# Optimization experiments

Hardware: AMD Instinct MI355X
Metric: run time of the kernel (lower is better)

The kernel has to match this reference:

```python
import jax, jax.numpy as jnp
import numpy as np

N_NODES = 250000
N_EDGES = 8000000


def _gcn_prep(edge_index, n):
    # PyG GCNConv default: add self-loops, symmetric normalization
    row = jnp.concatenate([edge_index[0], jnp.arange(n, dtype=edge_index.dtype)])
    col = jnp.concatenate([edge_index[1], jnp.arange(n, dtype=edge_index.dtype)])
    deg = jax.ops.segment_sum(jnp.ones_like(col, dtype=jnp.float32), col, num_segments=n)
    dinv = jnp.where(deg > 0, jax.lax.rsqrt(deg), 0.0)
    norm = dinv[row] * dinv[col]  # [E + N]
    return row, col, norm


def _gcn_conv(x, W, b, row, col, norm, n):
    h = x @ W  # transform first (small dense GEMM)
    msg = h[row] * norm[:, None]  # gather + per-edge scale
    out = jax.ops.segment_sum(msg, col, num_segments=n)  # scatter-add aggregate
    return out + b


def setup_inputs() -> dict:
    key = jax.random.key(0)
    ks = jax.random.split(key, 8)
    x = jax.random.normal(ks[0], (N_NODES, 2), dtype=jnp.float32)
    y1 = jax.random.normal(ks[1], (N_NODES,), dtype=jnp.float32)
    edge_index = jax.random.randint(ks[2], (2, N_EDGES), 0, N_NODES, dtype=jnp.int64)
    s = lambda fan_in: 1.0 / np.sqrt(fan_in)
    W1 = jax.random.uniform(ks[3], (3, 32), jnp.float32, -s(3), s(3))
    b1 = jnp.zeros((32,), jnp.float32)
    W2 = jax.random.uniform(ks[4], (32, 32), jnp.float32, -s(32), s(32))
    b2 = jnp.zeros((32,), jnp.float32)
    W3 = jax.random.uniform(ks[5], (32, 1), jnp.float32, -s(32), s(32))
    b3 = jnp.zeros((32,), jnp.float32)  # only b3[:1] is used (out_channels=1)
    return {"x": x, "y1": y1, "edge_index": edge_index,
            "W1": W1, "b1": b1, "W2": W2, "b2": b2, "W3": W3, "b3": b3}


def reference(x, y1, edge_index, W1, b1, W2, b2, W3, b3):
    n = x.shape[0]
    row, col, norm = _gcn_prep(edge_index, n)
    h = jnp.concatenate([x, y1[:, None]], axis=1)  # [N, 3]
    h = jax.nn.relu(_gcn_conv(h, W1, b1, row, col, norm, n))
    h = jax.nn.relu(_gcn_conv(h, W2, b2, row, col, norm, n))
    h = _gcn_conv(h, W3, b3[:1], row, col, norm, n)
    return h.reshape(-1)
```

## Files before the change

### kernel.cpp

```cpp
#include <hip/hip_runtime.h>
#include <stdint.h>

#define BSH 7
#define BW  128
#define MAXBUK 2048
#define SSH 13
#define SBW 8192
#define MAXSB 64
#define CMAX 4096

__global__ void k_hist(const int* __restrict__ ei, int E, int nbuk, int* __restrict__ bcnt) {
    __shared__ int h[MAXBUK];
    for (int b = threadIdx.x; b < nbuk; b += blockDim.x) h[b] = 0;
    __syncthreads();
    int stride = gridDim.x * blockDim.x;
    for (int e = blockIdx.x * blockDim.x + threadIdx.x; e < E; e += stride)
        atomicAdd(&h[ei[E + e] >> BSH], 1);
    __syncthreads();
    for (int b = threadIdx.x; b < nbuk; b += blockDim.x)
        if (h[b]) atomicAdd(&bcnt[b], h[b]);
}

__global__ void k_scan(const int* __restrict__ bcnt, int nbuk, int E, int nsb,
                       int* __restrict__ bbase, int* __restrict__ cursor,
                       int* __restrict__ sbase, int* __restrict__ scursor) {
    __shared__ int s0[MAXBUK], s1[MAXBUK];
    int tid = threadIdx.x;
    for (int i = tid; i < MAXBUK; i += blockDim.x) s0[i] = (i < nbuk) ? bcnt[i] : 0;
    __syncthreads();
    int* src = s0; int* dst = s1;
    for (int off = 1; off < MAXBUK; off <<= 1) {
        for (int i = tid; i < MAXBUK; i += blockDim.x)
            dst[i] = src[i] + ((i >= off) ? src[i - off] : 0);
        __syncthreads();
        int* t = src; src = dst; dst = t;
    }
    for (int i = tid; i < nbuk; i += blockDim.x) {
        int excl = src[i] - bcnt[i];
        bbase[i] = excl;
        cursor[i] = excl;
    }
    if (tid == 0) bbase[nbuk] = E;
    for (int i = tid; i <= nsb; i += blockDim.x) {
        int idx = i << 6;
        int v = (idx < nbuk) ? (src[idx] - bcnt[idx]) : E;
        sbase[i] = v;
        if (i < nsb) scursor[i] = v;
    }
}

__global__ void k_bin1(const int* __restrict__ ei, int E,
                       int* __restrict__ scursor, unsigned int* __restrict__ tmp) {
    __shared__ int colc[CMAX];
    __shared__ int h[MAXSB], base[MAXSB];
    int start = (int)blockIdx.x * CMAX;
    int end = min(start + CMAX, E);
    int cnt = end - start;
    if (threadIdx.x < MAXSB) h[threadIdx.x] = 0;
    __syncthreads();
    for (int i = threadIdx.x; i < cnt; i += blockDim.x) {
        int c = ei[E + start + i];
        colc[i] = c;
        atomicAdd(&h[c >> SSH], 1);
    }
    __syncthreads();
    if (threadIdx.x < MAXSB) {
        int c = h[threadIdx.x];
        base[threadIdx.x] = c ? atomicAdd(&scursor[threadIdx.x], c) : 0;
        h[threadIdx.x] = 0;
    }
    __syncthreads();
    for (int i = threadIdx.x; i < cnt; i += blockDim.x) {
        int r = ei[start + i];
        int c = colc[i];
        int sb = c >> SSH;
        int loc = atomicAdd(&h[sb], 1);
        tmp[base[sb] + loc] = ((unsigned)r << SSH) | (unsigned)(c & (SBW - 1));
    }
}

__global__ void k_bin2(const unsigned int* __restrict__ tmp, const int* __restrict__ sbase,
                       int* __restrict__ cursor, unsigned int* __restrict__ pairs) {
    __shared__ unsigned int cache[CMAX];
    __shared__ int h[64], base[64];
    int sb = blockIdx.x;
    int s = sbase[sb], e = sbase[sb + 1];
    int cnt = e - s;
    int chunk = (cnt + (int)gridDim.y - 1) / (int)gridDim.y;
    int start = s + (int)blockIdx.y * chunk;
    int end = min(start + chunk, e);
    int m = max(0, end - start);
    if (threadIdx.x < 64) h[threadIdx.x] = 0;
    __syncthreads();
    for (int i = threadIdx.x; i < m; i += blockDim.x) {
        unsigned v = tmp[start + i];
        cache[i] = v;
        atomicAdd(&h[(v & (SBW - 1u)) >> BSH], 1);
    }
    __syncthreads();
    if (threadIdx.x < 64) {
        int c = h[threadIdx.x];
        int fine = (sb << 6) + threadIdx.x;
        base[threadIdx.x] = c ? atomicAdd(&cursor[fine], c) : 0;
        h[threadIdx.x] = 0;
    }
    __syncthreads();
    for (int i = threadIdx.x; i < m; i += blockDim.x) {
        unsigned v = cache[i];
        unsigned colLow = v & (SBW - 1u);
        int lb = (int)(colLow >> BSH);
        int loc = atomicAdd(&h[lb], 1);
        pairs[base[lb] + loc] = ((v >> SSH) << BSH) | (colLow & (BW - 1u));
    }
}

__global__ void k_dcnt(const unsigned int* __restrict__ pairs, const int* __restrict__ bbase,
                       const float* __restrict__ x, const float* __restrict__ y1, int n,
                       float* __restrict__ dinv, float4* __restrict__ s4) {
    __shared__ int cnt[BW];
    int b = blockIdx.x;
    if (threadIdx.x < BW) cnt[threadIdx.x] = 0;
    __syncthreads();
    int s = bbase[b], e = bbase[b + 1];
    for (int j = s + threadIdx.x; j < e; j += blockDim.x)
        atomicAdd(&cnt[pairs[j] & (BW - 1u)], 1);
    __syncthreads();
    if (threadIdx.x < BW) {
        int col = (b << BSH) + threadIdx.x;
        if (col < n) {
            float d = rsqrtf((float)cnt[threadIdx.x] + 1.0f);
            dinv[col] = d;
            s4[col] = make_float4(d * x[2 * col], d * x[2 * col + 1], d * y1[col], d);
        }
    }
}

__global__ void k_L1(const unsigned int* __restrict__ pairs, const int* __restrict__ bbase,
                     const float4* __restrict__ s4, const float* __restrict__ W1,
                     const float* __restrict__ b1, const float* __restrict__ W2,
                     float* __restrict__ hs2, int n) {
    __shared__ double acc[BW * 3];
    int b = blockIdx.x;
    for (int i = threadIdx.x; i < BW * 3; i += blockDim.x) acc[i] = 0.0;
    __syncthreads();
    int s = bbase[b], e = bbase[b + 1];
    int j = s + threadIdx.x * 4;
    int stride = blockDim.x * 4;
    for (; j + 3 < e; j += stride) {
        unsigned pk0 = pairs[j], pk1 = pairs[j + 1], pk2 = pairs[j + 2], pk3 = pairs[j + 3];
        float4 v0 = s4[pk0 >> BSH];
        float4 v1 = s4[pk1 >> BSH];
        float4 v2 = s4[pk2 >> BSH];
        float4 v3 = s4[pk3 >> BSH];
        int c0 = (int)(pk0 & (BW - 1u)) * 3, c1 = (int)(pk1 & (BW - 1u)) * 3;
        int c2 = (int)(pk2 & (BW - 1u)) * 3, c3 = (int)(pk3 & (BW - 1u)) * 3;
        atomicAdd(&acc[c0 + 0], (double)v0.x);
        atomicAdd(&acc[c0 + 1], (double)v0.y);
        atomicAdd(&acc[c0 + 2], (double)v0.z);
        atomicAdd(&acc[c1 + 0], (double)v1.x);
        atomicAdd(&acc[c1 + 1], (double)v1.y);
        atomicAdd(&acc[c1 + 2], (double)v1.z);
        atomicAdd(&acc[c2 + 0], (double)v2.x);
        atomicAdd(&acc[c2 + 1], (double)v2.y);
        atomicAdd(&acc[c2 + 2], (double)v2.z);
        atomicAdd(&acc[c3 + 0], (double)v3.x);
        atomicAdd(&acc[c3 + 1], (double)v3.y);
        atomicAdd(&acc[c3 + 2], (double)v3.z);
    }
    if (j < e) {
        int lim = min(j + 4, e);
        for (int t = j; t < lim; ++t) {
            unsigned pk = pairs[t];
            float4 v = s4[pk >> BSH];
            int c = (int)(pk & (BW - 1u)) * 3;
            atomicAdd(&acc[c + 0], (double)v.x);
            atomicAdd(&acc[c + 1], (double)v.y);
            atomicAdd(&acc[c + 2], (double)v.z);
        }
    }
    __syncthreads();
    int f = threadIdx.x & 31;
    int g = threadIdx.x >> 5;
    for (int ci = g; ci < BW; ci += 8) {
        int col = (b << BSH) + ci;
        if (col >= n) continue;
        float4 sc = s4[col];
        float a0 = (float)acc[ci * 3 + 0] + sc.x;
        float a1 = (float)acc[ci * 3 + 1] + sc.y;
        float a2 = (float)acc[ci * 3 + 2] + sc.z;
        float d = sc.w;
        float t = a0 * W1[f] + a1 * W1[32 + f] + a2 * W1[64 + f];
        float h1 = fmaxf(d * t + b1[f], 0.0f);
        float o = 0.0f;
#pragma unroll
        for (int k = 0; k < 32; ++k)
            o += __shfl(h1, k, 32) * W2[k * 32 + f];
        hs2[(size_t)col * 32 + f] = d * o;
    }
}

__global__ void k_L2(const unsigned int* __restrict__ pairs, const int* __restrict__ bbase,
                     const float* __restrict__ hs2, const float* __restrict__ dinv,
                     const float* __restrict__ b2, const float* __restrict__ W3,
                     float* __restrict__ hs3, int n) {
    __shared__ double acc[BW * 32];
    int b = blockIdx.x;
    for (int i = threadIdx.x; i < BW * 32; i += blockDim.x) acc[i] = 0.0;
    __syncthreads();
    int s = bbase[b], e = bbase[b + 1];
    int f = threadIdx.x & 31;
    int g = threadIdx.x >> 5;
    int j = s + (g << 3);
    for (; j + 7 < e; j += 128) {
        unsigned pk0 = pairs[j],     pk1 = pairs[j + 1], pk2 = pairs[j + 2], pk3 = pairs[j + 3];
        unsigned pk4 = pairs[j + 4], pk5 = pairs[j + 5], pk6 = pairs[j + 6], pk7 = pairs[j + 7];
        float v0 = hs2[(size_t)(pk0 >> BSH) * 32 + f];
        float v1 = hs2[(size_t)(pk1 >> BSH) * 32 + f];
        float v2 = hs2[(size_t)(pk2 >> BSH) * 32 + f];
        float v3 = hs2[(size_t)(pk3 >> BSH) * 32 + f];
        float v4 = hs2[(size_t)(pk4 >> BSH) * 32 + f];
        float v5 = hs2[(size_t)(pk5 >> BSH) * 32 + f];
        float v6 = hs2[(size_t)(pk6 >> BSH) * 32 + f];
        float v7 = hs2[(size_t)(pk7 >> BSH) * 32 + f];
        atomicAdd(&acc[(pk0 & (BW - 1u)) * 32 + f], (double)v0);
        atomicAdd(&acc[(pk1 & (BW - 1u)) * 32 + f], (double)v1);
        atomicAdd(&acc[(pk2 & (BW - 1u)) * 32 + f], (double)v2);
        atomicAdd(&acc[(pk3 & (BW - 1u)) * 32 + f], (double)v3);
        atomicAdd(&acc[(pk4 & (BW - 1u)) * 32 + f], (double)v4);
        atomicAdd(&acc[(pk5 & (BW - 1u)) * 32 + f], (double)v5);
        atomicAdd(&acc[(pk6 & (BW - 1u)) * 32 + f], (double)v6);
        atomicAdd(&acc[(pk7 & (BW - 1u)) * 32 + f], (double)v7);
    }
    if (j < e) {
        int lim = min(j + 8, e);
        for (int t = j; t < lim; ++t) {
            unsigned pk = pairs[t];
            float v = hs2[(size_t)(pk >> BSH) * 32 + f];
            atomicAdd(&acc[(pk & (BW - 1u)) * 32 + f], (double)v);
        }
    }
    __syncthreads();
    for (int ci = g; ci < BW; ci += 16) {
        int col = (b << BSH) + ci;
        if (col >= n) continue;
        float d = dinv[col];
        float h2 = fmaxf(d * ((float)acc[ci * 32 + f] + hs2[(size_t)col * 32 + f]) + b2[f], 0.0f);
        float w = h2 * W3[f];
        for (int off = 16; off > 0; off >>= 1) w += __shfl_down(w, off, 32);
        if (f == 0) hs3[col] = d * w;
    }
}

__global__ void k_L3(const unsigned int* __restrict__ pairs, const int* __restrict__ bbase,
                     const float* __restrict__ hs3, const float* __restrict__ dinv,
                     const float* __restrict__ b3, float* __restrict__ out, int n) {
    __shared__ double acc[BW];
    int b = blockIdx.x;
    if (threadIdx.x < BW) acc[threadIdx.x] = 0.0;
    __syncthreads();
    int s = bbase[b], e = bbase[b + 1];
    int j = s + threadIdx.x * 4;
    int stride = blockDim.x * 4;
    for (; j + 3 < e; j += stride) {
        unsigned pk0 = pairs[j], pk1 = pairs[j + 1], pk2 = pairs[j + 2], pk3 = pairs[j + 3];
        float v0 = hs3[pk0 >> BSH];
        float v1 = hs3[pk1 >> BSH];
        float v2 = hs3[pk2 >> BSH];
        float v3 = hs3[pk3 >> BSH];
        atomicAdd(&acc[pk0 & (BW - 1u)], (double)v0);
        atomicAdd(&acc[pk1 & (BW - 1u)], (double)v1);
        atomicAdd(&acc[pk2 & (BW - 1u)], (double)v2);
        atomicAdd(&acc[pk3 & (BW - 1u)], (double)v3);
    }
    if (j < e) {
        int lim = min(j + 4, e);
        for (int t = j; t < lim; ++t) {
            unsigned pk = pairs[t];
            atomicAdd(&acc[pk & (BW - 1u)], (double)hs3[pk >> BSH]);
        }
    }
    __syncthreads();
    int col = (b << BSH) + threadIdx.x;
    if (threadIdx.x < BW && col < n)
        out[col] = dinv[col] * ((float)acc[threadIdx.x] + hs3[col]) + b3[0];
}


extern "C" void kernel_launch(void* const* d_in, const int* in_sizes, int n_in,
                              void* d_out, int out_size, void* d_ws, size_t ws_size,
                              hipStream_t stream) {
    const float* x  = (const float*)d_in[0];
    const float* y1 = (const float*)d_in[1];
    const int*   ei = (const int*)d_in[2];
    const float* W1 = (const float*)d_in[3];
    const float* b1 = (const float*)d_in[4];
    const float* W2 = (const float*)d_in[5];
    const float* b2 = (const float*)d_in[6];
    const float* W3 = (const float*)d_in[7];
    const float* b3 = (const float*)d_in[8];
    float* out = (float*)d_out;

    const int n = in_sizes[1];
    const int E = in_sizes[2] / 2;
    const int nbuk = (n + BW - 1) >> BSH;
    const int nsb = (nbuk + 63) >> 6;

    char* ws = (char*)d_ws;
    size_t off = 0;
    auto alloc = [&](size_t bytes) { char* p = ws + off; off += (bytes + 255) & ~(size_t)255; return p; };
    unsigned int* pairs = (unsigned int*)alloc((size_t)E * sizeof(unsigned int));
    float*  hs2   = (float*)alloc((size_t)n * 32 * sizeof(float));
    float4* s4    = (float4*)alloc((size_t)n * sizeof(float4));
    float*  dinv  = (float*)alloc((size_t)n * sizeof(float));
    float*  hs3   = (float*)alloc((size_t)n * sizeof(float));
    int*    bcnt  = (int*)alloc((size_t)nbuk * sizeof(int));
    int*    bbase = (int*)alloc((size_t)(nbuk + 1) * sizeof(int));
    int*    cursor= (int*)alloc((size_t)nbuk * sizeof(int));
    int*    sbase = (int*)alloc((size_t)(nsb + 1) * sizeof(int));
    int*    scursor = (int*)alloc((size_t)nsb * sizeof(int));
    (void)ws_size;
    unsigned int* tmp = (unsigned int*)hs2;

    hipMemsetAsync(bcnt, 0, (size_t)nbuk * sizeof(int), stream);
    k_hist<<<1024, 256, 0, stream>>>(ei, E, nbuk, bcnt);
    k_scan<<<1, 1024, 0, stream>>>(bcnt, nbuk, E, nsb, bbase, cursor, sbase, scursor);

    const int nbin1 = (E + CMAX - 1) / CMAX;
    k_bin1<<<nbin1, 256, 0, stream>>>(ei, E, scursor, tmp);
    k_bin2<<<dim3(nsb, 72), 256, 0, stream>>>(tmp, sbase, cursor, pairs);

    k_dcnt<<<nbuk, 256, 0, stream>>>(pairs, bbase, x, y1, n, dinv, s4);

    k_L1<<<nbuk, 256, 0, stream>>>(pairs, bbase, s4, W1, b1, W2, hs2, n);
    k_L2<<<nbuk, 512, 0, stream>>>(pairs, bbase, hs2, dinv, b2, W3, hs3, n);
    k_L3<<<nbuk, 256, 0, stream>>>(pairs, bbase, hs3, dinv, b3, out, n);
}
```

Before: 406.5 us.

## Build full CSR by destination and aggregate per node without shared atomics

Result: slower. 476.3 us (+17.2%).

```diff
diff --git a/kernel.cpp b/kernel.cpp
--- a/kernel.cpp
+++ b/kernel.cpp
@@ -114,175 +114,121 @@
     }
 }
 
-__global__ void k_dcnt(const unsigned int* __restrict__ pairs, const int* __restrict__ bbase,
-                       const float* __restrict__ x, const float* __restrict__ y1, int n,
+__global__ void k_sort(const unsigned int* __restrict__ pairs, const int* __restrict__ bbase,
+                       const float* __restrict__ x, const float* __restrict__ y1, int n, int E,
+                       int* __restrict__ rows, int* __restrict__ colptr,
                        float* __restrict__ dinv, float4* __restrict__ s4) {
     __shared__ int cnt[BW];
+    __shared__ int cbase[BW];
     int b = blockIdx.x;
+    int s = bbase[b], e = bbase[b + 1];
     if (threadIdx.x < BW) cnt[threadIdx.x] = 0;
     __syncthreads();
-    int s = bbase[b], e = bbase[b + 1];
     for (int j = s + threadIdx.x; j < e; j += blockDim.x)
         atomicAdd(&cnt[pairs[j] & (BW - 1u)], 1);
     __syncthreads();
+    if (threadIdx.x < BW) cbase[threadIdx.x] = cnt[threadIdx.x];
+    __syncthreads();
+    for (int off = 1; off < BW; off <<= 1) {
+        int v = 0;
+        if (threadIdx.x < BW && threadIdx.x >= off) v = cbase[threadIdx.x - off];
+        __syncthreads();
+        if (threadIdx.x < BW) cbase[threadIdx.x] += v;
+        __syncthreads();
+    }
     if (threadIdx.x < BW) {
+        int excl = cbase[threadIdx.x] - cnt[threadIdx.x];
         int col = (b << BSH) + threadIdx.x;
         if (col < n) {
+            colptr[col] = s + excl;
             float d = rsqrtf((float)cnt[threadIdx.x] + 1.0f);
             dinv[col] = d;
             s4[col] = make_float4(d * x[2 * col], d * x[2 * col + 1], d * y1[col], d);
         }
-    }
-}
-
-__global__ void k_L1(const unsigned int* __restrict__ pairs, const int* __restrict__ bbase,
+        cnt[threadIdx.x] = excl;
+    }
+    if (b == 0 && threadIdx.x == 0) colptr[n] = E;
+    __syncthreads();
+    for (int j = s + threadIdx.x; j < e; j += blockDim.x) {
+        unsigned pk = pairs[j];
+        int pos = atomicAdd(&cnt[pk & (BW - 1u)], 1);
+        rows[s + pos] = (int)(pk >> BSH);
+    }
+}
+
+__global__ void k_L1(const int* __restrict__ rows, const int* __restrict__ colptr,
                      const float4* __restrict__ s4, const float* __restrict__ W1,
                      const float* __restrict__ b1, const float* __restrict__ W2,
                      float* __restrict__ hs2, int n) {
-    __shared__ double acc[BW * 3];
-    int b = blockIdx.x;
-    for (int i = threadIdx.x; i < BW * 3; i += blockDim.x) acc[i] = 0.0;
-    __syncthreads();
-    int s = bbase[b], e = bbase[b + 1];
-    int j = s + threadIdx.x * 4;
-    int stride = blockDim.x * 4;
-    for (; j + 3 < e; j += stride) {
-        unsigned pk0 = pairs[j], pk1 = pairs[j + 1], pk2 = pairs[j + 2], pk3 = pairs[j + 3];
-        float4 v0 = s4[pk0 >> BSH];
-        float4 v1 = s4[pk1 >> BSH];
-        float4 v2 = s4[pk2 >> BSH];
-        float4 v3 = s4[pk3 >> BSH];
-        int c0 = (int)(pk0 & (BW - 1u)) * 3, c1 = (int)(pk1 & (BW - 1u)) * 3;
-        int c2 = (int)(pk2 & (BW - 1u)) * 3, c3 = (int)(pk3 & (BW - 1u)) * 3;
-        atomicAdd(&acc[c0 + 0], (double)v0.x);
-        atomicAdd(&acc[c0 + 1], (double)v0.y);
-        atomicAdd(&acc[c0 + 2], (double)v0.z);
-        atomicAdd(&acc[c1 + 0], (double)v1.x);
-        atomicAdd(&acc[c1 + 1], (double)v1.y);
-        atomicAdd(&acc[c1 + 2], (double)v1.z);
-        atomicAdd(&acc[c2 + 0], (double)v2.x);
-        atomicAdd(&acc[c2 + 1], (double)v2.y);
-        atomicAdd(&acc[c2 + 2], (double)v2.z);
-        atomicAdd(&acc[c3 + 0], (double)v3.x);
-        atomicAdd(&acc[c3 + 1], (double)v3.y);
-        atomicAdd(&acc[c3 + 2], (double)v3.z);
-    }
-    if (j < e) {
-        int lim = min(j + 4, e);
-        for (int t = j; t < lim; ++t) {
-            unsigned pk = pairs[t];
-            float4 v = s4[pk >> BSH];
-            int c = (int)(pk & (BW - 1u)) * 3;
-            atomicAdd(&acc[c + 0], (double)v.x);
-            atomicAdd(&acc[c + 1], (double)v.y);
-            atomicAdd(&acc[c + 2], (double)v.z);
-        }
-    }
-    __syncthreads();
-    int f = threadIdx.x & 31;
-    int g = threadIdx.x >> 5;
-    for (int ci = g; ci < BW; ci += 8) {
-        int col = (b << BSH) + ci;
-        if (col >= n) continue;
-        float4 sc = s4[col];
-        float a0 = (float)acc[ci * 3 + 0] + sc.x;
-        float a1 = (float)acc[ci * 3 + 1] + sc.y;
-        float a2 = (float)acc[ci * 3 + 2] + sc.z;
-        float d = sc.w;
-        float t = a0 * W1[f] + a1 * W1[32 + f] + a2 * W1[64 + f];
-        float h1 = fmaxf(d * t + b1[f], 0.0f);
-        float o = 0.0f;
-#pragma unroll
-        for (int k = 0; k < 32; ++k)
-            o += __shfl(h1, k, 32) * W2[k * 32 + f];
-        hs2[(size_t)col * 32 + f] = d * o;
-    }
-}
-
-__global__ void k_L2(const unsigned int* __restrict__ pairs, const int* __restrict__ bbase,
+    int t = blockIdx.x * blockDim.x + threadIdx.x;
+    int g = t >> 5, f = t & 31;
+    if (g >= n) return;
+    int s = colptr[g], e = colptr[g + 1];
+    double a0 = 0.0, a1 = 0.0, a2 = 0.0;
+    for (int j = s + f; j < e; j += 32) {
+        float4 v = s4[rows[j]];
+        a0 += (double)v.x; a1 += (double)v.y; a2 += (double)v.z;
+    }
+#pragma unroll
+    for (int off = 16; off > 0; off >>= 1) {
+        a0 += __shfl_xor(a0, off, 32);
+        a1 += __shfl_xor(a1, off, 32);
+        a2 += __shfl_xor(a2, off, 32);
+    }
+    float4 sc = s4[g];
+    float A0 = (float)a0 + sc.x;
+    float A1 = (float)a1 + sc.y;
+    float A2 = (float)a2 + sc.z;
+    float d = sc.w;
+    float h1 = fmaxf(d * (A0 * W1[f] + A1 * W1[32 + f] + A2 * W1[64 + f]) + b1[f], 0.0f);
+    float o = 0.0f;
+#pragma unroll
+    for (int k = 0; k < 32; ++k)
+        o += __shfl(h1, k, 32) * W2[k * 32 + f];
+    hs2[(size_t)g * 32 + f] = d * o;
+}
+
+__global__ void k_L2(const int* __restrict__ rows, const int* __restrict__ colptr,
                      const float* __restrict__ hs2, const float* __restrict__ dinv,
                      const float* __restrict__ b2, const float* __restrict__ W3,
                      float* __restrict__ hs3, int n) {
-    __shared__ double acc[BW * 32];
-    int b = blockIdx.x;
-    for (int i = threadIdx.x; i < BW * 32; i += blockDim.x) acc[i] = 0.0;
-    __syncthreads();
-    int s = bbase[b], e = bbase[b + 1];
-    int f = threadIdx.x & 31;
-    int g = threadIdx.x >> 5;
-    int j = s + (g << 3);
-    for (; j + 7 < e; j += 128) {
-        unsigned pk0 = pairs[j],     pk1 = pairs[j + 1], pk2 = pairs[j + 2], pk3 = pairs[j + 3];
-        unsigned pk4 = pairs[j + 4], pk5 = pairs[j + 5], pk6 = pairs[j + 6], pk7 = pairs[j + 7];
-        float v0 = hs2[(size_t)(pk0 >> BSH) * 32 + f];
-        float v1 = hs2[(size_t)(pk1 >> BSH) * 32 + f];
-        float v2 = hs2[(size_t)(pk2 >> BSH) * 32 + f];
-        float v3 = hs2[(size_t)(pk3 >> BSH) * 32 + f];
-        float v4 = hs2[(size_t)(pk4 >> BSH) * 32 + f];
-        float v5 = hs2[(size_t)(pk5 >> BSH) * 32 + f];
-        float v6 = hs2[(size_t)(pk6 >> BSH) * 32 + f];
-        float v7 = hs2[(size_t)(pk7 >> BSH) * 32 + f];
-        atomicAdd(&acc[(pk0 & (BW - 1u)) * 32 + f], (double)v0);
-        atomicAdd(&acc[(pk1 & (BW - 1u)) * 32 + f], (double)v1);
-        atomicAdd(&acc[(pk2 & (BW - 1u)) * 32 + f], (double)v2);
-        atomicAdd(&acc[(pk3 & (BW - 1u)) * 32 + f], (double)v3);
-        atomicAdd(&acc[(pk4 & (BW - 1u)) * 32 + f], (double)v4);
-        atomicAdd(&acc[(pk5 & (BW - 1u)) * 32 + f], (double)v5);
-        atomicAdd(&acc[(pk6 & (BW - 1u)) * 32 + f], (double)v6);
-        atomicAdd(&acc[(pk7 & (BW - 1u)) * 32 + f], (double)v7);
-    }
-    if (j < e) {
-        int lim = min(j + 8, e);
-        for (int t = j; t < lim; ++t) {
-            unsigned pk = pairs[t];
-            float v = hs2[(size_t)(pk >> BSH) * 32 + f];
-            atomicAdd(&acc[(pk & (BW - 1u)) * 32 + f], (double)v);
-        }
-    }
-    __syncthreads();
-    for (int ci = g; ci < BW; ci += 16) {
-        int col = (b << BSH) + ci;
-        if (col >= n) continue;
-        float d = dinv[col];
-        float h2 = fmaxf(d * ((float)acc[ci * 32 + f] + hs2[(size_t)col * 32 + f]) + b2[f], 0.0f);
-        float w = h2 * W3[f];
-        for (int off = 16; off > 0; off >>= 1) w += __shfl_down(w, off, 32);
-        if (f == 0) hs3[col] = d * w;
-    }
-}
-
-__global__ void k_L3(const unsigned int* __restrict__ pairs, const int* __restrict__ bbase,
+    int t = blockIdx.x * blockDim.x + threadIdx.x;
+    int g = t >> 5, f = t & 31;
+    if (g >= n) return;
+    int s = colptr[g], e = colptr[g + 1];
+    double acc = 0.0;
+    int j = s;
+    for (; j + 7 < e; j += 8) {
+        int r0 = rows[j],     r1 = rows[j + 1], r2 = rows[j + 2], r3 = rows[j + 3];
+        int r4 = rows[j + 4], r5 = rows[j + 5], r6 = rows[j + 6], r7 = rows[j + 7];
+        float v0 = hs2[(size_t)r0 * 32 + f], v1 = hs2[(size_t)r1 * 32 + f];
+        float v2 = hs2[(size_t)r2 * 32 + f], v3 = hs2[(size_t)r3 * 32 + f];
+        float v4 = hs2[(size_t)r4 * 32 + f], v5 = hs2[(size_t)r5 * 32 + f];
+        float v6 = hs2[(size_t)r6 * 32 + f], v7 = hs2[(size_t)r7 * 32 + f];
+        acc += (((double)v0 + (double)v1) + ((double)v2 + (double)v3))
+             + (((double)v4 + (double)v5) + ((double)v6 + (double)v7));
+    }
+    for (; j < e; ++j) acc += (double)hs2[(size_t)rows[j] * 32 + f];
+    float d = dinv[g];
+    float h2 = fmaxf(d * ((float)acc + hs2[(size_t)g * 32 + f]) + b2[f], 0.0f);
+    float w = h2 * W3[f];
+#pragma unroll
+    for (int off = 16; off > 0; off >>= 1) w += __shfl_down(w, off, 32);
+    if (f == 0) hs3[g] = d * w;
+}
+
+__global__ void k_L3(const int* __restrict__ rows, const int* __restrict__ colptr,
                      const float* __restrict__ hs3, const float* __restrict__ dinv,
                      const float* __restrict__ b3, float* __restrict__ out, int n) {
-    __shared__ double acc[BW];
-    int b = blockIdx.x;
-    if (threadIdx.x < BW) acc[threadIdx.x] = 0.0;
-    __syncthreads();
-    int s = bbase[b], e = bbase[b + 1];
-    int j = s + threadIdx.x * 4;
-    int stride = blockDim.x * 4;
-    for (; j + 3 < e; j += stride) {
-        unsigned pk0 = pairs[j], pk1 = pairs[j + 1], pk2 = pairs[j + 2], pk3 = pairs[j + 3];
-        float v0 = hs3[pk0 >> BSH];
-        float v1 = hs3[pk1 >> BSH];
-        float v2 = hs3[pk2 >> BSH];
-        float v3 = hs3[pk3 >> BSH];
-        atomicAdd(&acc[pk0 & (BW - 1u)], (double)v0);
-        atomicAdd(&acc[pk1 & (BW - 1u)], (double)v1);
-        atomicAdd(&acc[pk2 & (BW - 1u)], (double)v2);
-        atomicAdd(&acc[pk3 & (BW - 1u)], (double)v3);
-    }
-    if (j < e) {
-        int lim = min(j + 4, e);
-        for (int t = j; t < lim; ++t) {
-            unsigned pk = pairs[t];
-            atomicAdd(&acc[pk & (BW - 1u)], (double)hs3[pk >> BSH]);
-        }
-    }
-    __syncthreads();
-    int col = (b << BSH) + threadIdx.x;
-    if (threadIdx.x < BW && col < n)
-        out[col] = dinv[col] * ((float)acc[threadIdx.x] + hs3[col]) + b3[0];
+    int t = blockIdx.x * blockDim.x + threadIdx.x;
+    int g = t >> 5, l = t & 31;
+    if (g >= n) return;
+    int s = colptr[g], e = colptr[g + 1];
+    double acc = 0.0;
+    for (int j = s + l; j < e; j += 32) acc += (double)hs3[rows[j]];
+#pragma unroll
+    for (int off = 16; off > 0; off >>= 1) acc += __shfl_down(acc, off, 32);
+    if (l == 0) out[g] = dinv[g] * ((float)acc + hs3[g]) + b3[0];
 }
 
 
@@ -309,17 +255,19 @@
     size_t off = 0;
     auto alloc = [&](size_t bytes) { char* p = ws + off; off += (bytes + 255) & ~(size_t)255; return p; };
     unsigned int* pairs = (unsigned int*)alloc((size_t)E * sizeof(unsigned int));
+    int*    rows  = (int*)alloc((size_t)E * sizeof(int));
     float*  hs2   = (float*)alloc((size_t)n * 32 * sizeof(float));
     float4* s4    = (float4*)alloc((size_t)n * sizeof(float4));
     float*  dinv  = (float*)alloc((size_t)n * sizeof(float));
     float*  hs3   = (float*)alloc((size_t)n * sizeof(float));
+    int*    colptr= (int*)alloc((size_t)(n + 1) * sizeof(int));
     int*    bcnt  = (int*)alloc((size_t)nbuk * sizeof(int));
     int*    bbase = (int*)alloc((size_t)(nbuk + 1) * sizeof(int));
     int*    cursor= (int*)alloc((size_t)nbuk * sizeof(int));
     int*    sbase = (int*)alloc((size_t)(nsb + 1) * sizeof(int));
     int*    scursor = (int*)alloc((size_t)nsb * sizeof(int));
     (void)ws_size;
-    unsigned int* tmp = (unsigned int*)hs2;
+    unsigned int* tmp = (unsigned int*)rows;
 
     hipMemsetAsync(bcnt, 0, (size_t)nbuk * sizeof(int), stream);
     k_hist<<<1024, 256, 0, stream>>>(ei, E, nbuk, bcnt);
@@ -328,10 +276,10 @@
     const int nbin1 = (E + CMAX - 1) / CMAX;
     k_bin1<<<nbin1, 256, 0, stream>>>(ei, E, scursor, tmp);
     k_bin2<<<dim3(nsb, 72), 256, 0, stream>>>(tmp, sbase, cursor, pairs);
-
-    k_dcnt<<<nbuk, 256, 0, stream>>>(pairs, bbase, x, y1, n, dinv, s4);
-
-    k_L1<<<nbuk, 256, 0, stream>>>(pairs, bbase, s4, W1, b1, W2, hs2, n);
-    k_L2<<<nbuk, 512, 0, stream>>>(pairs, bbase, hs2, dinv, b2, W3, hs3, n);
-    k_L3<<<nbuk, 256, 0, stream>>>(pairs, bbase, hs3, dinv, b3, out, n);
-}
+    k_sort<<<nbuk, 256, 0, stream>>>(pairs, bbase, x, y1, n, E, rows, colptr, dinv, s4);
+
+    const int gGrp = (n * 32 + 511) / 512;
+    k_L1<<<gGrp, 512, 0, stream>>>(rows, colptr, s4, W1, b1, W2, hs2, n);
+    k_L2<<<gGrp, 512, 0, stream>>>(rows, colptr, hs2, dinv, b2, W3, hs3, n);
+    k_L3<<<gGrp, 512, 0, stream>>>(rows, colptr, hs3, dinv, b3, out, n);
+}
```

## Split layer-2 feature table into halves mapped to separate XCD groups

Applied to the files above, without the earlier changes.

Result: slower. 499.1 us (+22.8%).

```diff
diff --git a/kernel.cpp b/kernel.cpp
--- a/kernel.cpp
+++ b/kernel.cpp
@@ -138,7 +138,7 @@
 __global__ void k_L1(const unsigned int* __restrict__ pairs, const int* __restrict__ bbase,
                      const float4* __restrict__ s4, const float* __restrict__ W1,
                      const float* __restrict__ b1, const float* __restrict__ W2,
-                     float* __restrict__ hs2, int n) {
+                     float* __restrict__ hs2a, float* __restrict__ hs2b, int n) {
     __shared__ double acc[BW * 3];
     int b = blockIdx.x;
     for (int i = threadIdx.x; i < BW * 3; i += blockDim.x) acc[i] = 0.0;
@@ -195,59 +195,70 @@
 #pragma unroll
         for (int k = 0; k < 32; ++k)
             o += __shfl(h1, k, 32) * W2[k * 32 + f];
-        hs2[(size_t)col * 32 + f] = d * o;
+        float val = d * o;
+        if (f < 16) hs2a[(size_t)col * 16 + f] = val;
+        else        hs2b[(size_t)col * 16 + (f - 16)] = val;
     }
 }
 
 __global__ void k_L2(const unsigned int* __restrict__ pairs, const int* __restrict__ bbase,
-                     const float* __restrict__ hs2, const float* __restrict__ dinv,
-                     const float* __restrict__ b2, const float* __restrict__ W3,
-                     float* __restrict__ hs3, int n) {
-    __shared__ double acc[BW * 32];
-    int b = blockIdx.x;
-    for (int i = threadIdx.x; i < BW * 32; i += blockDim.x) acc[i] = 0.0;
+                     const float* __restrict__ hs2a, const float* __restrict__ hs2b,
+                     const float* __restrict__ dinv, const float* __restrict__ b2,
+                     const float* __restrict__ W3, float* __restrict__ hs3,
+                     int nbuk, int n) {
+    __shared__ double acc[BW * 16];
+    int bid = (int)blockIdx.x;
+    int xcd = bid & 7;
+    int half = xcd >> 2;
+    int b = (bid >> 3) * 4 + (xcd & 3);
+    if (b >= nbuk) return;
+    const float* __restrict__ T = half ? hs2b : hs2a;
+    for (int i = threadIdx.x; i < BW * 16; i += blockDim.x) acc[i] = 0.0;
     __syncthreads();
     int s = bbase[b], e = bbase[b + 1];
-    int f = threadIdx.x & 31;
-    int g = threadIdx.x >> 5;
+    int f = threadIdx.x & 15;
+    int g = threadIdx.x >> 4;
     int j = s + (g << 3);
     for (; j + 7 < e; j += 128) {
         unsigned pk0 = pairs[j],     pk1 = pairs[j + 1], pk2 = pairs[j + 2], pk3 = pairs[j + 3];
         unsigned pk4 = pairs[j + 4], pk5 = pairs[j + 5], pk6 = pairs[j + 6], pk7 = pairs[j + 7];
-        float v0 = hs2[(size_t)(pk0 >> BSH) * 32 + f];
-        float v1 = hs2[(size_t)(pk1 >> BSH) * 32 + f];
-        float v2 = hs2[(size_t)(pk2 >> BSH) * 32 + f];
-        float v3 = hs2[(size_t)(pk3 >> BSH) * 32 + f];
-        float v4 = hs2[(size_t)(pk4 >> BSH) * 32 + f];
-        float v5 = hs2[(size_t)(pk5 >> BSH) * 32 + f];
-        float v6 = hs2[(size_t)(pk6 >> BSH) * 32 + f];
-        float v7 = hs2[(size_t)(pk7 >> BSH) * 32 + f];
-        atomicAdd(&acc[(pk0 & (BW - 1u)) * 32 + f], (double)v0);
-        atomicAdd(&acc[(pk1 & (BW - 1u)) * 32 + f], (double)v1);
-        atomicAdd(&acc[(pk2 & (BW - 1u)) * 32 + f], (double)v2);
-        atomicAdd(&acc[(pk3 & (BW - 1u)) * 32 + f], (double)v3);
-        atomicAdd(&acc[(pk4 & (BW - 1u)) * 32 + f], (double)v4);
-        atomicAdd(&acc[(pk5 & (BW - 1u)) * 32 + f], (double)v5);
-        atomicAdd(&acc[(pk6 & (BW - 1u)) * 32 + f], (double)v6);
-        atomicAdd(&acc[(pk7 & (BW - 1u)) * 32 + f], (double)v7);
+        float v0 = T[(size_t)(pk0 >> BSH) * 16 + f];
+        float v1 = T[(size_t)(pk1 >> BSH) * 16 + f];
+        float v2 = T[(size_t)(pk2 >> BSH) * 16 + f];
+        float v3 = T[(size_t)(pk3 >> BSH) * 16 + f];
+        float v4 = T[(size_t)(pk4 >> BSH) * 16 + f];
+        float v5 = T[(size_t)(pk5 >> BSH) * 16 + f];
+        float v6 = T[(size_t)(pk6 >> BSH) * 16 + f];
+        float v7 = T[(size_t)(pk7 >> BSH) * 16 + f];
+        atomicAdd(&acc[(pk0 & (BW - 1u)) * 16 + f], (double)v0);
+        atomicAdd(&acc[(pk1 & (BW - 1u)) * 16 + f], (double)v1);
+        atomicAdd(&acc[(pk2 & (BW - 1u)) * 16 + f], (double)v2);
+        atomicAdd(&acc[(pk3 & (BW - 1u)) * 16 + f], (double)v3);
+        atomicAdd(&acc[(pk4 & (BW - 1u)) * 16 + f], (double)v4);
+        atomicAdd(&acc[(pk5 & (BW - 1u)) * 16 + f], (double)v5);
+        atomicAdd(&acc[(pk6 & (BW - 1u)) * 16 + f], (double)v6);
+        atomicAdd(&acc[(pk7 & (BW - 1u)) * 16 + f], (double)v7);
     }
     if (j < e) {
         int lim = min(j + 8, e);
         for (int t = j; t < lim; ++t) {
             unsigned pk = pairs[t];
-            float v = hs2[(size_t)(pk >> BSH) * 32 + f];
-            atomicAdd(&acc[(pk & (BW - 1u)) * 32 + f], (double)v);
+            float v = T[(size_t)(pk >> BSH) * 16 + f];
+            atomicAdd(&acc[(pk & (BW - 1u)) * 16 + f], (double)v);
         }
     }
     __syncthreads();
+    float w3 = W3[(half << 4) + f];
+    float bb = b2[(half << 4) + f];
     for (int ci = g; ci < BW; ci += 16) {
         int col = (b << BSH) + ci;
         if (col >= n) continue;
         float d = dinv[col];
-        float h2 = fmaxf(d * ((float)acc[ci * 32 + f] + hs2[(size_t)col * 32 + f]) + b2[f], 0.0f);
-        float w = h2 * W3[f];
-        for (int off = 16; off > 0; off >>= 1) w += __shfl_down(w, off, 32);
-        if (f == 0) hs3[col] = d * w;
+        float h2 = fmaxf(d * ((float)acc[ci * 16 + f] + T[(size_t)col * 16 + f]) + bb, 0.0f);
+        float w = h2 * w3;
+#pragma unroll
+        for (int off = 8; off > 0; off >>= 1) w += __shfl_down(w, off, 16);
+        if (f == 0) atomicAdd(&hs3[col], d * w);
     }
 }
 
@@ -309,7 +320,8 @@
     size_t off = 0;
     auto alloc = [&](size_t bytes) { char* p = ws + off; off += (bytes + 255) & ~(size_t)255; return p; };
     unsigned int* pairs = (unsigned int*)alloc((size_t)E * sizeof(unsigned int));
-    float*  hs2   = (float*)alloc((size_t)n * 32 * sizeof(float));
+    float*  hs2a  = (float*)alloc((size_t)n * 16 * sizeof(float));
+    float*  hs2b  = (float*)alloc((size_t)n * 16 * sizeof(float));
     float4* s4    = (float4*)alloc((size_t)n * sizeof(float4));
     float*  dinv  = (float*)alloc((size_t)n * sizeof(float));
     float*  hs3   = (float*)alloc((size_t)n * sizeof(float));
@@ -319,7 +331,7 @@
     int*    sbase = (int*)alloc((size_t)(nsb + 1) * sizeof(int));
     int*    scursor = (int*)alloc((size_t)nsb * sizeof(int));
     (void)ws_size;
-    unsigned int* tmp = (unsigned int*)hs2;
+    unsigned int* tmp = (unsigned int*)hs2a;
 
     hipMemsetAsync(bcnt, 0, (size_t)nbuk * sizeof(int), stream);
     k_hist<<<1024, 256, 0, stream>>>(ei, E, nbuk, bcnt);
@@ -331,7 +343,9 @@
 
     k_dcnt<<<nbuk, 256, 0, stream>>>(pairs, bbase, x, y1, n, dinv, s4);
 
-    k_L1<<<nbuk, 256, 0, stream>>>(pairs, bbase, s4, W1, b1, W2, hs2, n);
-    k_L2<<<nbuk, 512, 0, stream>>>(pairs, bbase, hs2, dinv, b2, W3, hs3, n);
+    k_L1<<<nbuk, 256, 0, stream>>>(pairs, bbase, s4, W1, b1, W2, hs2a, hs2b, n);
+    hipMemsetAsync(hs3, 0, (size_t)n * sizeof(float), stream);
+    const int gL2 = ((nbuk + 3) / 4) * 8;
+    k_L2<<<gL2, 256, 0, stream>>>(pairs, bbase, hs2a, hs2b, dinv, b2, W3, hs3, nbuk, n);
     k_L3<<<nbuk, 256, 0, stream>>>(pairs, bbase, hs3, dinv, b3, out, n);
 }
```
